# Kernel tuning notes

Hardware: AMD Instinct MI355X
Metric: run time of the kernel (lower is better)

The kernel has to match this reference:

```python
import jax, jax.numpy as jnp
import numpy as np

KH, KW = 2, 2  # kernel_size; stride == kernel_size (default), pad == 0 for this config

def setup_inputs() -> dict:
    key = jax.random.key(0)
    k1, k2 = jax.random.split(key)
    B, C, H, W = 32, 64, 64, 64
    nH, nW = H // KH, W // KW
    L = nH * nW                     # 1024
    n = KH * KW * C                 # 256 (grouping = in_feature)
    x = jax.random.normal(k1, (B, C, H, W), dtype=jnp.float32)
    stdv = 6.0 / np.sqrt(n * n / 1.0) ** 0.5  # placeholder, recomputed below
    stdv = 6.0 / np.sqrt(float(n * n) / 1.0) if False else 6.0 / np.sqrt(float(n) * float(n) / float(n)) / 1.0
    stdv = 6.0 / np.sqrt(float(n * n))  # numel // L == n*n -> stdv = 6/sqrt(n*n) = 6/n
    weight = jax.random.uniform(k2, (L, n, n), dtype=jnp.float32, minval=-stdv, maxval=stdv)
    bias = jnp.zeros((1, 1, n, L), dtype=jnp.float32)
    return {"x": x, "weight": weight, "bias": bias}

def reference(x, weight, bias):
    # PointConv with kernel=(2,2), stride=(2,2), pad=0, grouping=C.
    B, C, H, W = x.shape
    nH, nW = H // KH, W // KW
    L = nH * nW
    n = C * KH * KW
    # F.unfold (non-overlapping, stride==kernel): channel order (c, kh, kw), L order (ph, pw)
    patches = x.reshape(B, C, nH, KH, nW, KW).transpose(0, 1, 3, 5, 2, 4).reshape(B, n, L)
    p = patches.reshape(B, 1, n, L)  # (B, C//grouping=1, n, L)
    # per-location matmul: distinct [n,n] weight per spatial patch l
    m = jnp.einsum('bcnl,lnp->bcpl', p, weight) + bias  # (B,1,n,L)
    m = m.reshape(B, C, KH, KW, nH, nW)
    # F.fold inverse of the unfold above
    out = m.transpose(0, 1, 4, 2, 5, 3).reshape(B, C, H, W)
    return out
```

## Files before the change

### kernel.cpp

```cpp
#include <hip/hip_runtime.h>


#define B_  32
#define C_  64
#define H_  64
#define W_  64
#define L_  1024
#define N_  256
#define SA  264

typedef __bf16 bf16x8 __attribute__((ext_vector_type(8)));
typedef float  f32x4  __attribute__((ext_vector_type(4)));

__device__ __forceinline__ unsigned short f2bf(float f) {
  unsigned int u = __builtin_bit_cast(unsigned int, f);
  u += 0x7FFFu + ((u >> 16) & 1u);
  return (unsigned short)(u >> 16);
}

__global__ __launch_bounds__(256, 3) void pointconv_kernel(
    const float* __restrict__ x, const float* __restrict__ wgt,
    const float* __restrict__ bias, float* __restrict__ out) {
  __shared__ unsigned short A[B_ * SA];

  const int bid = blockIdx.x;
  const int l  = ((bid & 7) << 7) | (bid >> 3);
  const int ph = l >> 5, pw = l & 31;
  const int h0 = ph * 2, w0 = pw * 2;
  const int tid = threadIdx.x;

  const float* __restrict__ wl = wgt + (size_t)l * (N_ * N_);

  const int lane = tid & 63;
  const int wv   = tid >> 6;
  const int col  = lane & 15;
  const int quad = lane >> 4;

  const float* __restrict__ wp = wl + (quad * 8) * N_ + wv * 64 + col;

  float rb0[4][8], rb1[4][8];

#pragma unroll
  for (int nt = 0; nt < 4; ++nt)
#pragma unroll
    for (int j = 0; j < 8; ++j)
      rb0[nt][j] = wp[j * N_ + nt * 16];

  {
    const int b  = tid & 31;
    const int c0 = tid >> 5;
#pragma unroll
    for (int i = 0; i < 8; ++i) {
      const int c = c0 + i * 8;
      const float* px = x + (((b * C_ + c) * H_ + h0) * W_ + w0);
      float2 v0 = *(const float2*)px;
      float2 v1 = *(const float2*)(px + W_);
      ushort4 q;
      q.x = f2bf(v0.x); q.y = f2bf(v0.y);
      q.z = f2bf(v1.x); q.w = f2bf(v1.y);
      *(ushort4*)&A[b * SA + c * 4] = q;
    }
  }

  f32x4 acc[2][4];
#pragma unroll
  for (int nt = 0; nt < 4; ++nt) {
    const int p = wv * 64 + nt * 16 + col;
    const float bv = bias[p * L_ + l];
#pragma unroll
    for (int mt = 0; mt < 2; ++mt) {
      acc[mt][nt][0] = bv; acc[mt][nt][1] = bv;
      acc[mt][nt][2] = bv; acc[mt][nt][3] = bv;
    }
  }

  __syncthreads();

#pragma unroll
  for (int s = 0; s < 8; ++s) {
    if (s < 7) {
      const float* np = wp + (s + 1) * 32 * N_;
      if (s & 1) {
#pragma unroll
        for (int nt = 0; nt < 4; ++nt)
#pragma unroll
          for (int j = 0; j < 8; ++j)
            rb0[nt][j] = np[j * N_ + nt * 16];
      } else {
#pragma unroll
        for (int nt = 0; nt < 4; ++nt)
#pragma unroll
          for (int j = 0; j < 8; ++j)
            rb1[nt][j] = np[j * N_ + nt * 16];
      }
    }

    bf16x8 af[2];
#pragma unroll
    for (int mt = 0; mt < 2; ++mt)
      af[mt] = *(const bf16x8*)&A[(mt * 16 + col) * SA + s * 32 + quad * 8];

#pragma unroll
    for (int nt = 0; nt < 4; ++nt) {
      union { unsigned short u[8]; bf16x8 v; } bu;
#pragma unroll
      for (int j = 0; j < 8; ++j)
        bu.u[j] = f2bf((s & 1) ? rb1[nt][j] : rb0[nt][j]);
#pragma unroll
      for (int mt = 0; mt < 2; ++mt)
        acc[mt][nt] = __builtin_amdgcn_mfma_f32_16x16x32_bf16(
            af[mt], bu.v, acc[mt][nt], 0, 0, 0);
    }
  }

#pragma unroll
  for (int mt = 0; mt < 2; ++mt) {
#pragma unroll
    for (int nt = 0; nt < 4; ++nt) {
      const int p  = wv * 64 + nt * 16 + col;
      const int c  = p >> 2;
      const int kh = (p >> 1) & 1;
      const int kw = p & 1;
      float* po = out + (((c * H_) + h0 + kh) * W_ + w0 + kw);
#pragma unroll
      for (int r = 0; r < 4; ++r) {
        const int b = mt * 16 + quad * 4 + r;
        po[b * (C_ * H_ * W_)] = acc[mt][nt][r];
      }
    }
  }
}

extern "C" void kernel_launch(void* const* d_in, const int* in_sizes, int n_in,
                              void* d_out, int out_size, void* d_ws, size_t ws_size,
                              hipStream_t stream) {
  const float* x    = (const float*)d_in[0];
  const float* wgt  = (const float*)d_in[1];
  const float* bias = (const float*)d_in[2];
  float* out = (float*)d_out;
  pointconv_kernel<<<dim3(L_), dim3(256), 0, stream>>>(x, wgt, bias, out);
}
```

Measured before the change: 438.3 us.

## Split each patch's output columns across two blocks and drop register double-buffering

```diff
diff --git a/kernel.cpp b/kernel.cpp
--- a/kernel.cpp
+++ b/kernel.cpp
@@ -18,33 +18,25 @@
   return (unsigned short)(u >> 16);
 }
 
-__global__ __launch_bounds__(256, 3) void pointconv_kernel(
+__global__ __launch_bounds__(256, 8) void pointconv_kernel(
     const float* __restrict__ x, const float* __restrict__ wgt,
     const float* __restrict__ bias, float* __restrict__ out) {
   __shared__ unsigned short A[B_ * SA];
 
   const int bid = blockIdx.x;
-  const int l  = ((bid & 7) << 7) | (bid >> 3);
+  const int l    = ((bid & 7) << 7) | (bid >> 4);
+  const int half = (bid >> 3) & 1;
   const int ph = l >> 5, pw = l & 31;
   const int h0 = ph * 2, w0 = pw * 2;
-  const int tid = threadIdx.x;
-
-  const float* __restrict__ wl = wgt + (size_t)l * (N_ * N_);
-
+  const int tid  = threadIdx.x;
   const int lane = tid & 63;
   const int wv   = tid >> 6;
   const int col  = lane & 15;
   const int quad = lane >> 4;
 
-  const float* __restrict__ wp = wl + (quad * 8) * N_ + wv * 64 + col;
-
-  float rb0[4][8], rb1[4][8];
-
-#pragma unroll
-  for (int nt = 0; nt < 4; ++nt)
-#pragma unroll
-    for (int j = 0; j < 8; ++j)
-      rb0[nt][j] = wp[j * N_ + nt * 16];
+  const int pbase = half * 128 + wv * 32;
+  const float* __restrict__ wl = wgt + (size_t)l * (N_ * N_);
+  const float* __restrict__ wp = wl + (quad * 8) * N_ + pbase + col;
 
   {
     const int b  = tid & 31;
@@ -62,11 +54,10 @@
     }
   }
 
-  f32x4 acc[2][4];
+  f32x4 acc[2][2];
 #pragma unroll
-  for (int nt = 0; nt < 4; ++nt) {
-    const int p = wv * 64 + nt * 16 + col;
-    const float bv = bias[p * L_ + l];
+  for (int nt = 0; nt < 2; ++nt) {
+    const float bv = bias[(pbase + nt * 16 + col) * L_ + l];
 #pragma unroll
     for (int mt = 0; mt < 2; ++mt) {
       acc[mt][nt][0] = bv; acc[mt][nt][1] = bv;
@@ -78,46 +69,27 @@
 
 #pragma unroll
   for (int s = 0; s < 8; ++s) {
-    if (s < 7) {
-      const float* np = wp + (s + 1) * 32 * N_;
-      if (s & 1) {
+    bf16x8 af0 = *(const bf16x8*)&A[col * SA + s * 32 + quad * 8];
+    bf16x8 af1 = *(const bf16x8*)&A[(16 + col) * SA + s * 32 + quad * 8];
 #pragma unroll
-        for (int nt = 0; nt < 4; ++nt)
-#pragma unroll
-          for (int j = 0; j < 8; ++j)
-            rb0[nt][j] = np[j * N_ + nt * 16];
-      } else {
-#pragma unroll
-        for (int nt = 0; nt < 4; ++nt)
-#pragma unroll
-          for (int j = 0; j < 8; ++j)
-            rb1[nt][j] = np[j * N_ + nt * 16];
-      }
-    }
-
-    bf16x8 af[2];
-#pragma unroll
-    for (int mt = 0; mt < 2; ++mt)
-      af[mt] = *(const bf16x8*)&A[(mt * 16 + col) * SA + s * 32 + quad * 8];
-
-#pragma unroll
-    for (int nt = 0; nt < 4; ++nt) {
+    for (int nt = 0; nt < 2; ++nt) {
+      const float* wr = wp + (size_t)(s * 32) * N_ + nt * 16;
       union { unsigned short u[8]; bf16x8 v; } bu;
 #pragma unroll
       for (int j = 0; j < 8; ++j)
-        bu.u[j] = f2bf((s & 1) ? rb1[nt][j] : rb0[nt][j]);
-#pragma unroll
-      for (int mt = 0; mt < 2; ++mt)
-        acc[mt][nt] = __builtin_amdgcn_mfma_f32_16x16x32_bf16(
-            af[mt], bu.v, acc[mt][nt], 0, 0, 0);
+        bu.u[j] = f2bf(wr[j * N_]);
+      acc[0][nt] = __builtin_amdgcn_mfma_f32_16x16x32_bf16(af0, bu.v,
+                                                           acc[0][nt], 0, 0, 0);
+      acc[1][nt] = __builtin_amdgcn_mfma_f32_16x16x32_bf16(af1, bu.v,
+                                                           acc[1][nt], 0, 0, 0);
     }
   }
 
 #pragma unroll
   for (int mt = 0; mt < 2; ++mt) {
 #pragma unroll
-    for (int nt = 0; nt < 4; ++nt) {
-      const int p  = wv * 64 + nt * 16 + col;
+    for (int nt = 0; nt < 2; ++nt) {
+      const int p  = pbase + nt * 16 + col;
       const int c  = p >> 2;
       const int kh = (p >> 1) & 1;
       const int kw = p & 1;
@@ -138,5 +110,5 @@
   const float* wgt  = (const float*)d_in[1];
   const float* bias = (const float*)d_in[2];
   float* out = (float*)d_out;
-  pointconv_kernel<<<dim3(L_), dim3(256), 0, stream>>>(x, wgt, bias, out);
+  pointconv_kernel<<<dim3(2 * L_), dim3(256), 0, stream>>>(x, wgt, bias, out);
 }
```

Result: slower. 455.9 us (+4.0%).
